# Kernel tuning notes

Hardware: AMD Instinct MI355X
Metric: run time of the kernel (lower is better)

Reference implementation:

```python
import jax, jax.numpy as jnp
import numpy as np

DIM = 256
HEADS = 8
WS = 7          # window_size
WN = 8          # window_num per side
H = W = WS * WN # 56
B = 32
MLP_HIDDEN = 4 * DIM
SCALE = (DIM // HEADS) ** -0.5
LN_EPS = 1e-5


def _rel_index(ws):
    # pairwise relative position index inside a ws x ws window (dense 0..(2ws-1)^2-1,
    # so remap_position_index is the identity relabeling)
    ch, cw = np.meshgrid(np.arange(ws), np.arange(ws), indexing='ij')
    cf = np.stack([ch.ravel(), cw.ravel()])            # (2, ws*ws)
    rel = cf[:, :, None] - cf[:, None, :]              # (2, N, N)
    rel = rel.transpose(1, 2, 0).astype(np.int32)
    rel[..., 0] += ws - 1
    rel[..., 1] += ws - 1
    rel[..., 0] *= 2 * ws - 1
    return rel.sum(-1)                                 # (N, N) in [0, (2ws-1)^2)


def _layernorm(x, g, b):
    m = x.mean(-1, keepdims=True)
    v = ((x - m) ** 2).mean(-1, keepdims=True)
    return (x - m) * jax.lax.rsqrt(v + LN_EPS) * g + b


def _mhsa(x, qkv_w, qkv_b, proj_w, proj_b, bias):
    # x: (B_, N, C); bias: (nH, N, N) or None
    B_, N, C = x.shape
    hd = C // HEADS
    qkv = (x @ qkv_w.T + qkv_b).reshape(B_, N, 3, HEADS, hd).transpose(2, 0, 3, 1, 4)
    q, k, v = qkv[0], qkv[1], qkv[2]
    attn = jnp.einsum('bhqd,bhkd->bhqk', q * SCALE, k)
    if bias is not None:
        attn = attn + bias[None]
    attn = jax.nn.softmax(attn, axis=-1)
    out = jnp.einsum('bhqk,bhkd->bhqd', attn, v).transpose(0, 2, 1, 3).reshape(B_, N, C)
    return out @ proj_w.T + proj_b


def setup_inputs() -> dict:
    key = jax.random.key(0)
    ks = jax.random.split(key, 8)
    f32 = jnp.float32
    return {
        'regional_tokens': jax.random.normal(ks[0], (B, WN * WN, DIM), f32),
        'x': jax.random.normal(ks[1], (B, H * W, DIM), f32),
        'norm1_g': jnp.ones((DIM,), f32), 'norm1_b': jnp.zeros((DIM,), f32),
        'norm2_g': jnp.ones((DIM,), f32), 'norm2_b': jnp.zeros((DIM,), f32),
        'norm3_g': jnp.ones((DIM,), f32), 'norm3_b': jnp.zeros((DIM,), f32),
        'qkv_w': jax.random.normal(ks[2], (3 * DIM, DIM), f32) * 0.02,
        'qkv_b': jnp.zeros((3 * DIM,), f32),
        'proj_w': jax.random.normal(ks[3], (DIM, DIM), f32) * 0.02,
        'proj_b': jnp.zeros((DIM,), f32),
        'bias_table': jax.random.normal(ks[4], ((2 * WS - 1) ** 2, HEADS), f32) * 0.02,
        'fc1_w': jax.random.normal(ks[5], (MLP_HIDDEN, DIM), f32) * 0.02,
        'fc1_b': jnp.zeros((MLP_HIDDEN,), f32),
        'fc2_w': jax.random.normal(ks[6], (DIM, MLP_HIDDEN), f32) * 0.02,
        'fc2_b': jnp.zeros((DIM,), f32),
        'rel_index': jnp.asarray(_rel_index(WS)),
    }


def reference(regional_tokens, x, norm1_g, norm1_b, norm2_g, norm2_b, norm3_g, norm3_b,
              qkv_w, qkv_b, proj_w, proj_b, bias_table, fc1_w, fc1_b, fc2_w, fc2_b,
              rel_index):
    Bb, L, C = x.shape
    nW = regional_tokens.shape[1]
    ws2 = WS * WS
    # --- RSA: attention over regional tokens (no relative bias) ---
    regional_tokens = regional_tokens + _mhsa(
        _layernorm(regional_tokens, norm1_g, norm1_b), qkv_w, qkv_b, proj_w, proj_b, None)
    # --- window partition of x: (B,H,W,C) -> (nW*B, ws*ws, C) (batch-major) ---
    xw = x.reshape(Bb, H // WS, WS, W // WS, WS, C)
    xw = xw.transpose(0, 1, 3, 2, 4, 5).reshape(-1, ws2, C)
    # regional tokens reshaped window-major, exactly as the torch code does
    reg = regional_tokens.transpose(1, 0, 2).reshape(nW * Bb, 1, C)
    t = jnp.concatenate([reg, xw], axis=1)  # (nW*B, 1+ws2, C)
    # --- LSA relative position bias, zero-padded for the regional token ---
    bias = bias_table[rel_index]                       # (ws2, ws2, nH)
    bias = jnp.pad(bias, ((1, 0), (1, 0), (0, 0)))      # (1+ws2, 1+ws2, nH)
    bias = bias.transpose(2, 0, 1)                      # (nH, N, N)
    t = t + _mhsa(_layernorm(t, norm2_g, norm2_b), qkv_w, qkv_b, proj_w, proj_b, bias)
    # --- MLP ---
    h = _layernorm(t, norm3_g, norm3_b)
    h = jax.nn.gelu(h @ fc1_w.T + fc1_b, approximate=False) @ fc2_w.T + fc2_b
    t = t + h
    # --- split back ---
    reg_out = t[:, 0, :].reshape(nW, Bb, C).transpose(1, 0, 2)   # (B, nW, C)
    xw = t[:, 1:, :].reshape(Bb, H // WS, W // WS, WS, WS, C)
    x_out = xw.transpose(0, 1, 3, 2, 4, 5).reshape(Bb, L, C)
    return reg_out, x_out
```

## Files before the change

### kernel.cpp

```cpp
#include <hip/hip_runtime.h>
#include <math.h>

#define SCALE_Q 0.17677669529663687f

typedef __attribute__((ext_vector_type(8))) short bf16x8;
typedef __attribute__((ext_vector_type(4))) float f32x4;
typedef __attribute__((ext_vector_type(4))) unsigned short u16x4;

static __device__ __forceinline__ unsigned short f2bf(float f) {
    unsigned int u = __float_as_uint(f);
    u += 0x7FFF + ((u >> 16) & 1);
    return (unsigned short)(u >> 16);
}

static __device__ __forceinline__ float gelu_fast(float v) {
    float s = v * (0.7978845608f + 0.0356774081f * v * v);
    float e = __expf(-2.0f * s);
    return v * __builtin_amdgcn_rcpf(1.0f + e);
}

__global__ void prep_kernel(const float* __restrict__ qkv_w, const float* __restrict__ proj_w,
                            const float* __restrict__ fc1_w, const float* __restrict__ fc2_w,
                            const float* __restrict__ bias_table, const int* __restrict__ rel_index,
                            unsigned short* __restrict__ wq, unsigned short* __restrict__ wp,
                            unsigned short* __restrict__ w1, unsigned short* __restrict__ w2,
                            float* __restrict__ bias_pad) {
    int tid = blockIdx.x * blockDim.x + threadIdx.x;
    int stride = gridDim.x * blockDim.x;
    for (int i = tid; i < 768 * 256; i += stride) wq[i] = f2bf(qkv_w[i]);
    for (int i = tid; i < 256 * 256; i += stride) wp[i] = f2bf(proj_w[i]);
    for (int i = tid; i < 1024 * 256; i += stride) w1[i] = f2bf(fc1_w[i]);
    for (int i = tid; i < 256 * 1024; i += stride) w2[i] = f2bf(fc2_w[i]);
    for (int i = tid; i < 8 * 64 * 64; i += stride) {
        int h = i >> 12, q = (i >> 6) & 63, k = i & 63;
        float v;
        if (k >= 50) v = -1e30f;
        else if (q == 0 || k == 0 || q >= 50) v = 0.f;
        else v = bias_table[rel_index[(q - 1) * 49 + (k - 1)] * 8 + h];
        bias_pad[i] = v;
    }
}

template <int IS_RSA>
__global__ __launch_bounds__(1024, 4) void attn_kernel(
    const float* __restrict__ reg_tok, const float* __restrict__ x,
    const float* __restrict__ reg2_in, float* __restrict__ out,
    const float* __restrict__ ln_g, const float* __restrict__ ln_b,
    const unsigned short* __restrict__ wq, const float* __restrict__ qkv_b,
    const unsigned short* __restrict__ wp, const float* __restrict__ proj_b,
    const float* __restrict__ bias_pad) {
    __shared__ __align__(16) unsigned char smem[140288];
    unsigned short* regA = (unsigned short*)smem;
    unsigned short* regB = (unsigned short*)(smem + 36864);
    unsigned short* vT   = (unsigned short*)(smem + 103424);

    const int tid = threadIdx.x;
    const int lane = tid & 63;
    const int wid = tid >> 6;
    const int l15 = lane & 15;
    const int lg = lane >> 4;
    const int u = blockIdx.x;
    const int NV = IS_RSA ? 64 : 50;
    const f32x4 fzero = {0.f, 0.f, 0.f, 0.f};

    int reg_off = 0, xb = 0, wi = 0, wj = 0;
    if (!IS_RSA) {
        reg_off = ((u & 31) * 64 + (u >> 5)) * 256;
        xb = u >> 6;
        int xn = u & 63;
        wi = xn >> 3; wj = xn & 7;
    }

    for (int r = wid; r < 64; r += 16) {
        if (r < NV) {
            const float* src;
            if (IS_RSA) src = reg_tok + (u * 64 + r) * 256;
            else if (r == 0) src = reg2_in + reg_off;
            else {
                int p = r - 1;
                src = x + (xb * 3136 + (wi * 7 + p / 7) * 56 + (wj * 7 + p % 7)) * 256;
            }
            f32x4 v = *(const f32x4*)(src + lane * 4);
            float s = v[0] + v[1] + v[2] + v[3];
            float s2 = v[0] * v[0] + v[1] * v[1] + v[2] * v[2] + v[3] * v[3];
            #pragma unroll
            for (int m = 1; m < 64; m <<= 1) { s += __shfl_xor(s, m); s2 += __shfl_xor(s2, m); }
            float mean = s * 0.00390625f;
            float rstd = rsqrtf(s2 * 0.00390625f - mean * mean + 1e-5f);
            u16x4 o;
            #pragma unroll
            for (int j = 0; j < 4; ++j) {
                int c = lane * 4 + j;
                o[j] = f2bf((v[j] - mean) * rstd * ln_g[c] + ln_b[c]);
            }
            *(u16x4*)(regA + r * 264 + lane * 4) = o;
        } else {
            u16x4 z = {0, 0, 0, 0};
            *(u16x4*)(regA + r * 264 + lane * 4) = z;
        }
    }
    __syncthreads();

    const int h = wid >> 1;
    const int qb = (wid & 1) * 32;

    {
        f32x4 acc[4][3];
        #pragma unroll
        for (int mi = 0; mi < 4; ++mi)
            #pragma unroll
            for (int t = 0; t < 3; ++t) acc[mi][t] = fzero;
        #pragma unroll
        for (int ks = 0; ks < 8; ++ks) {
            int k = ks * 32 + lg * 8;
            bf16x8 a[4], b[3];
            #pragma unroll
            for (int mi = 0; mi < 4; ++mi) a[mi] = *(const bf16x8*)(regA + (mi * 16 + l15) * 264 + k);
            #pragma unroll
            for (int t = 0; t < 3; ++t) b[t] = *(const bf16x8*)(wq + (wid * 48 + t * 16 + l15) * 256 + k);
            #pragma unroll
            for (int mi = 0; mi < 4; ++mi)
                #pragma unroll
                for (int t = 0; t < 3; ++t)
                    acc[mi][t] = __builtin_amdgcn_mfma_f32_16x16x32_bf16(a[mi], b[t], acc[mi][t], 0, 0, 0);
        }
        #pragma unroll
        for (int mi = 0; mi < 4; ++mi)
            #pragma unroll
            for (int t = 0; t < 3; ++t) {
                int col = wid * 48 + t * 16 + l15;
                float bias = qkv_b[col];
                #pragma unroll
                for (int r = 0; r < 4; ++r) {
                    int row = mi * 16 + lg * 4 + r;
                    unsigned short hv = f2bf(acc[mi][t][r] + bias);
                    if (col < 512) regB[row * 520 + col] = hv;
                    else vT[(col - 512) * 72 + row] = hv;
                }
            }
    }

    f32x4 bv[4][2];
    if (!IS_RSA) {
        #pragma unroll
        for (int mi = 0; mi < 4; ++mi)
            #pragma unroll
            for (int nj = 0; nj < 2; ++nj)
                bv[mi][nj] = *(const f32x4*)(bias_pad + h * 4096 + (qb + nj * 16 + l15) * 64 + mi * 16 + lg * 4);
    }
    __syncthreads();

    f32x4 st[4][2];
    {
        int k0 = h * 32 + lg * 8;
        bf16x8 af[4], bfq[2];
        #pragma unroll
        for (int mi = 0; mi < 4; ++mi) af[mi] = *(const bf16x8*)(regB + (mi * 16 + l15) * 520 + 256 + k0);
        #pragma unroll
        for (int nj = 0; nj < 2; ++nj) bfq[nj] = *(const bf16x8*)(regB + (qb + nj * 16 + l15) * 520 + k0);
        #pragma unroll
        for (int mi = 0; mi < 4; ++mi)
            #pragma unroll
            for (int nj = 0; nj < 2; ++nj)
                st[mi][nj] = __builtin_amdgcn_mfma_f32_16x16x32_bf16(af[mi], bfq[nj], fzero, 0, 0, 0);
    }

    u16x4 pf[4][2];
    #pragma unroll
    for (int nj = 0; nj < 2; ++nj) {
        float ps[4][4];
        float mx = -3.0e38f;
        #pragma unroll
        for (int mi = 0; mi < 4; ++mi)
            #pragma unroll
            for (int r = 0; r < 4; ++r) {
                float t = st[mi][nj][r] * SCALE_Q;
                if (!IS_RSA) t += bv[mi][nj][r];
                ps[mi][r] = t;
                mx = fmaxf(mx, t);
            }
        mx = fmaxf(mx, __shfl_xor(mx, 16));
        mx = fmaxf(mx, __shfl_xor(mx, 32));
        float sum = 0.f;
        #pragma unroll
        for (int mi = 0; mi < 4; ++mi)
            #pragma unroll
            for (int r = 0; r < 4; ++r) { ps[mi][r] = __expf(ps[mi][r] - mx); sum += ps[mi][r]; }
        sum += __shfl_xor(sum, 16);
        sum += __shfl_xor(sum, 32);
        float inv = __builtin_amdgcn_rcpf(sum);
        #pragma unroll
        for (int mi = 0; mi < 4; ++mi) {
            u16x4 p4;
            #pragma unroll
            for (int r = 0; r < 4; ++r) p4[r] = f2bf(ps[mi][r] * inv);
            pf[mi][nj] = p4;
        }
    }

    f32x4 ov[2][2];
    #pragma unroll
    for (int m2 = 0; m2 < 2; ++m2) { ov[m2][0] = fzero; ov[m2][1] = fzero; }
    #pragma unroll
    for (int kt = 0; kt < 4; ++kt) {
        bf16x8 pb[2];
        #pragma unroll
        for (int nj = 0; nj < 2; ++nj) {
            bf16x8 t;
            t[0] = (short)pf[kt][nj][0]; t[1] = (short)pf[kt][nj][1];
            t[2] = (short)pf[kt][nj][2]; t[3] = (short)pf[kt][nj][3];
            t[4] = 0; t[5] = 0; t[6] = 0; t[7] = 0;
            pb[nj] = t;
        }
        #pragma unroll
        for (int m2 = 0; m2 < 2; ++m2) {
            u16x4 av = *(const u16x4*)(vT + (h * 32 + m2 * 16 + l15) * 72 + kt * 16 + lg * 4);
            bf16x8 a8;
            a8[0] = (short)av[0]; a8[1] = (short)av[1]; a8[2] = (short)av[2]; a8[3] = (short)av[3];
            a8[4] = 0; a8[5] = 0; a8[6] = 0; a8[7] = 0;
            #pragma unroll
            for (int nj = 0; nj < 2; ++nj)
                ov[m2][nj] = __builtin_amdgcn_mfma_f32_16x16x32_bf16(a8, pb[nj], ov[m2][nj], 0, 0, 0);
        }
    }
    #pragma unroll
    for (int m2 = 0; m2 < 2; ++m2)
        #pragma unroll
        for (int nj = 0; nj < 2; ++nj) {
            u16x4 o4;
            #pragma unroll
            for (int r = 0; r < 4; ++r) o4[r] = f2bf(ov[m2][nj][r]);
            *(u16x4*)(regA + (qb + nj * 16 + l15) * 264 + h * 32 + m2 * 16 + lg * 4) = o4;
        }
    __syncthreads();

    {
        int nb = wid * 16;
        f32x4 acc[4];
        #pragma unroll
        for (int mi = 0; mi < 4; ++mi) acc[mi] = fzero;
        #pragma unroll
        for (int ks = 0; ks < 8; ++ks) {
            int k = ks * 32 + lg * 8;
            bf16x8 a[4], b;
            #pragma unroll
            for (int mi = 0; mi < 4; ++mi) a[mi] = *(const bf16x8*)(regA + (mi * 16 + l15) * 264 + k);
            b = *(const bf16x8*)(wp + (nb + l15) * 256 + k);
            #pragma unroll
            for (int mi = 0; mi < 4; ++mi)
                acc[mi] = __builtin_amdgcn_mfma_f32_16x16x32_bf16(a[mi], b, acc[mi], 0, 0, 0);
        }
        int col = nb + l15;
        float pb = proj_b[col];
        #pragma unroll
        for (int mi = 0; mi < 4; ++mi)
            #pragma unroll
            for (int r = 0; r < 4; ++r) {
                int row = mi * 16 + lg * 4 + r;
                if (row < NV) {
                    float val = acc[mi][r] + pb;
                    if (IS_RSA) {
                        int off = (u * 64 + row) * 256 + col;
                        out[off] = val + reg_tok[off];
                    } else if (row == 0) {
                        out[reg_off + col] = val + reg2_in[reg_off + col];
                    } else {
                        int p = row - 1;
                        int off = (xb * 3136 + (wi * 7 + p / 7) * 56 + (wj * 7 + p % 7)) * 256 + col;
                        out[524288 + off] = val + x[off];
                    }
                }
            }
    }
}

__global__ __launch_bounds__(512, 4) void mlp_kernel(
    float* __restrict__ dout,
    const float* __restrict__ ln_g, const float* __restrict__ ln_b,
    const unsigned short* __restrict__ w1, const float* __restrict__ b1,
    const unsigned short* __restrict__ w2, const float* __restrict__ b2) {
    __shared__ __align__(16) unsigned short xst[64 * 264];
    __shared__ __align__(16) unsigned short hld[2][64 * 136];
    const int tid = threadIdx.x;
    const int lane = tid & 63;
    const int wid = tid >> 6;
    const int l15 = lane & 15;
    const int lg = lane >> 4;
    const int row0 = blockIdx.x * 64;
    const f32x4 fzero = {0.f, 0.f, 0.f, 0.f};

    #pragma unroll
    for (int i = 0; i < 8; ++i) {
        int r = wid * 8 + i;
        f32x4 v = *(const f32x4*)(dout + (row0 + r) * 256 + lane * 4);
        float s = v[0] + v[1] + v[2] + v[3];
        float s2 = v[0] * v[0] + v[1] * v[1] + v[2] * v[2] + v[3] * v[3];
        #pragma unroll
        for (int m = 1; m < 64; m <<= 1) { s += __shfl_xor(s, m); s2 += __shfl_xor(s2, m); }
        float mean = s * 0.00390625f;
        float rstd = rsqrtf(s2 * 0.00390625f - mean * mean + 1e-5f);
        u16x4 o;
        #pragma unroll
        for (int j = 0; j < 4; ++j) {
            int c = lane * 4 + j;
            o[j] = f2bf((v[j] - mean) * rstd * ln_g[c] + ln_b[c]);
        }
        *(u16x4*)(xst + r * 264 + lane * 4) = o;
    }

    bf16x8 w1f[8], w2f[8];
    #pragma unroll
    for (int ks = 0; ks < 8; ++ks)
        w1f[ks] = *(const bf16x8*)(w1 + (wid * 16 + l15) * 256 + ks * 32 + lg * 8);
    #pragma unroll
    for (int ks = 0; ks < 4; ++ks)
        #pragma unroll
        for (int ni = 0; ni < 2; ++ni)
            w2f[ks * 2 + ni] = *(const bf16x8*)(w2 + (wid * 32 + ni * 16 + l15) * 1024 + ks * 32 + lg * 8);
    __syncthreads();

    f32x4 acc2[4][2];
    #pragma unroll
    for (int mi = 0; mi < 4; ++mi) { acc2[mi][0] = fzero; acc2[mi][1] = fzero; }

    #pragma unroll
    for (int c = 0; c < 8; ++c) {
        unsigned short* hb = &hld[c & 1][0];
        f32x4 acc1[4];
        #pragma unroll
        for (int mi = 0; mi < 4; ++mi) acc1[mi] = fzero;
        #pragma unroll
        for (int ks = 0; ks < 8; ++ks) {
            int k = ks * 32 + lg * 8;
            bf16x8 a[4];
            #pragma unroll
            for (int mi = 0; mi < 4; ++mi)
                a[mi] = *(const bf16x8*)(xst + (mi * 16 + l15) * 264 + k);
            #pragma unroll
            for (int mi = 0; mi < 4; ++mi)
                acc1[mi] = __builtin_amdgcn_mfma_f32_16x16x32_bf16(a[mi], w1f[ks], acc1[mi], 0, 0, 0);
        }
        if (c < 7) {
            #pragma unroll
            for (int ks = 0; ks < 8; ++ks)
                w1f[ks] = *(const bf16x8*)(w1 + ((c + 1) * 128 + wid * 16 + l15) * 256 + ks * 32 + lg * 8);
        }
        {
            int hc = wid * 16 + l15;
            float bb = b1[c * 128 + hc];
            #pragma unroll
            for (int mi = 0; mi < 4; ++mi)
                #pragma unroll
                for (int r = 0; r < 4; ++r)
                    hb[(mi * 16 + lg * 4 + r) * 136 + hc] = f2bf(gelu_fast(acc1[mi][r] + bb));
        }
        __syncthreads();
        #pragma unroll
        for (int ks = 0; ks < 4; ++ks) {
            int k = ks * 32 + lg * 8;
            bf16x8 a[4];
            #pragma unroll
            for (int mi = 0; mi < 4; ++mi)
                a[mi] = *(const bf16x8*)(hb + (mi * 16 + l15) * 136 + k);
            #pragma unroll
            for (int mi = 0; mi < 4; ++mi)
                #pragma unroll
                for (int ni = 0; ni < 2; ++ni)
                    acc2[mi][ni] = __builtin_amdgcn_mfma_f32_16x16x32_bf16(a[mi], w2f[ks * 2 + ni], acc2[mi][ni], 0, 0, 0);
        }
        if (c < 7) {
            #pragma unroll
            for (int ks = 0; ks < 4; ++ks)
                #pragma unroll
                for (int ni = 0; ni < 2; ++ni)
                    w2f[ks * 2 + ni] = *(const bf16x8*)(w2 + (wid * 32 + ni * 16 + l15) * 1024 + (c + 1) * 128 + ks * 32 + lg * 8);
        }
    }
    #pragma unroll
    for (int mi = 0; mi < 4; ++mi)
        #pragma unroll
        for (int ni = 0; ni < 2; ++ni) {
            int col = wid * 32 + ni * 16 + l15;
            float bb = b2[col];
            #pragma unroll
            for (int r = 0; r < 4; ++r) {
                int row = row0 + mi * 16 + lg * 4 + r;
                float* dst = dout + row * 256 + col;
                *dst = acc2[mi][ni][r] + bb + *dst;
            }
        }
}

extern "C" void kernel_launch(void* const* d_in, const int* in_sizes, int n_in,
                              void* d_out, int out_size, void* d_ws, size_t ws_size,
                              hipStream_t stream) {
    const float* regional = (const float*)d_in[0];
    const float* x = (const float*)d_in[1];
    const float* n1g = (const float*)d_in[2];
    const float* n1b = (const float*)d_in[3];
    const float* n2g = (const float*)d_in[4];
    const float* n2b = (const float*)d_in[5];
    const float* n3g = (const float*)d_in[6];
    const float* n3b = (const float*)d_in[7];
    const float* qkvw = (const float*)d_in[8];
    const float* qkvb = (const float*)d_in[9];
    const float* projw = (const float*)d_in[10];
    const float* projb = (const float*)d_in[11];
    const float* btab = (const float*)d_in[12];
    const float* f1w = (const float*)d_in[13];
    const float* f1b = (const float*)d_in[14];
    const float* f2w = (const float*)d_in[15];
    const float* f2b = (const float*)d_in[16];
    const int* relidx = (const int*)d_in[17];

    unsigned char* ws = (unsigned char*)d_ws;
    unsigned short* wq = (unsigned short*)(ws);
    unsigned short* wp = (unsigned short*)(ws + 393216);
    unsigned short* w1 = (unsigned short*)(ws + 524288);
    unsigned short* w2 = (unsigned short*)(ws + 1048576);
    float* bias_pad    = (float*)(ws + 1572864);
    float* reg2        = (float*)(ws + 1703936);

    float* out = (float*)d_out;

    prep_kernel<<<512, 256, 0, stream>>>(qkvw, projw, f1w, f2w, btab, relidx, wq, wp, w1, w2, bias_pad);
    attn_kernel<1><<<32, 1024, 0, stream>>>(regional, x, nullptr, reg2, n1g, n1b, wq, qkvb, wp, projb, nullptr);
    attn_kernel<0><<<2048, 1024, 0, stream>>>(regional, x, reg2, out, n2g, n2b, wq, qkvb, wp, projb, bias_pad);
    mlp_kernel<<<1600, 512, 0, stream>>>(out, n3g, n3b, w1, f1b, w2, f2b);
}
```

Measured before the change: 485.4 us.

## Use LDS-only barriers, prefetch proj weights, and uniform-branch QKV scatter

Replaces __syncthreads with a custom barrier that waits only on LDS/scalar counters, so outstanding global loads (weight prefetches) need not drain at each barrier. Projection weights are prefetched into registers right after the QKV GEMM so their latency overlaps attention. The QKV store is split into wave-uniform branches by q/k versus v, removing per-element divergence. The w2 fragment loads move inside the MLP loop just before the barrier, lowering register pressure at the cost of less prefetch distance.

Result: slower. 498.4 us (+2.7%).

```diff
diff --git a/kernel.cpp b/kernel.cpp
--- a/kernel.cpp
+++ b/kernel.cpp
@@ -17,6 +17,12 @@
     float s = v * (0.7978845608f + 0.0356774081f * v * v);
     float e = __expf(-2.0f * s);
     return v * __builtin_amdgcn_rcpf(1.0f + e);
+}
+
+static __device__ __forceinline__ void barrier_lds_only() {
+    asm volatile("s_waitcnt lgkmcnt(0)" ::: "memory");
+    __builtin_amdgcn_s_barrier();
+    asm volatile("" ::: "memory");
 }
 
 __global__ void prep_kernel(const float* __restrict__ qkv_w, const float* __restrict__ proj_w,
@@ -57,6 +63,7 @@
     const int tid = threadIdx.x;
     const int lane = tid & 63;
     const int wid = tid >> 6;
+    const int widu = __builtin_amdgcn_readfirstlane(wid);
     const int l15 = lane & 15;
     const int lg = lane >> 4;
     const int u = blockIdx.x;
@@ -99,11 +106,12 @@
             *(u16x4*)(regA + r * 264 + lane * 4) = z;
         }
     }
-    __syncthreads();
+    barrier_lds_only();
 
     const int h = wid >> 1;
     const int qb = (wid & 1) * 32;
 
+    bf16x8 wpf[8];
     {
         f32x4 acc[4][3];
         #pragma unroll
@@ -125,19 +133,34 @@
                     acc[mi][t] = __builtin_amdgcn_mfma_f32_16x16x32_bf16(a[mi], b[t], acc[mi][t], 0, 0, 0);
         }
         #pragma unroll
-        for (int mi = 0; mi < 4; ++mi)
-            #pragma unroll
-            for (int t = 0; t < 3; ++t) {
-                int col = wid * 48 + t * 16 + l15;
-                float bias = qkv_b[col];
+        for (int ks = 0; ks < 8; ++ks)
+            wpf[ks] = *(const bf16x8*)(wp + (wid * 16 + l15) * 256 + ks * 32 + lg * 8);
+        #pragma unroll
+        for (int t = 0; t < 3; ++t) {
+            if (3 * widu + t < 32) {
                 #pragma unroll
-                for (int r = 0; r < 4; ++r) {
-                    int row = mi * 16 + lg * 4 + r;
-                    unsigned short hv = f2bf(acc[mi][t][r] + bias);
-                    if (col < 512) regB[row * 520 + col] = hv;
-                    else vT[(col - 512) * 72 + row] = hv;
+                for (int mi = 0; mi < 4; ++mi) {
+                    int col = wid * 48 + t * 16 + l15;
+                    float bias = qkv_b[col];
+                    #pragma unroll
+                    for (int r = 0; r < 4; ++r) {
+                        int row = mi * 16 + lg * 4 + r;
+                        regB[row * 520 + col] = f2bf(acc[mi][t][r] + bias);
+                    }
                 }
-            }
+            } else {
+                #pragma unroll
+                for (int mi = 0; mi < 4; ++mi) {
+                    int col = wid * 48 + t * 16 + l15;
+                    float bias = qkv_b[col];
+                    #pragma unroll
+                    for (int r = 0; r < 4; ++r) {
+                        int row = mi * 16 + lg * 4 + r;
+                        vT[(col - 512) * 72 + row] = f2bf(acc[mi][t][r] + bias);
+                    }
+                }
+            }
+        }
     }
 
     f32x4 bv[4][2];
@@ -148,7 +171,7 @@
             for (int nj = 0; nj < 2; ++nj)
                 bv[mi][nj] = *(const f32x4*)(bias_pad + h * 4096 + (qb + nj * 16 + l15) * 64 + mi * 16 + lg * 4);
     }
-    __syncthreads();
+    barrier_lds_only();
 
     f32x4 st[4][2];
     {
@@ -232,25 +255,23 @@
             for (int r = 0; r < 4; ++r) o4[r] = f2bf(ov[m2][nj][r]);
             *(u16x4*)(regA + (qb + nj * 16 + l15) * 264 + h * 32 + m2 * 16 + lg * 4) = o4;
         }
-    __syncthreads();
+    barrier_lds_only();
 
     {
-        int nb = wid * 16;
         f32x4 acc[4];
         #pragma unroll
         for (int mi = 0; mi < 4; ++mi) acc[mi] = fzero;
         #pragma unroll
         for (int ks = 0; ks < 8; ++ks) {
             int k = ks * 32 + lg * 8;
-            bf16x8 a[4], b;
+            bf16x8 a[4];
             #pragma unroll
             for (int mi = 0; mi < 4; ++mi) a[mi] = *(const bf16x8*)(regA + (mi * 16 + l15) * 264 + k);
-            b = *(const bf16x8*)(wp + (nb + l15) * 256 + k);
-            #pragma unroll
-            for (int mi = 0; mi < 4; ++mi)
-                acc[mi] = __builtin_amdgcn_mfma_f32_16x16x32_bf16(a[mi], b, acc[mi], 0, 0, 0);
-        }
-        int col = nb + l15;
+            #pragma unroll
+            for (int mi = 0; mi < 4; ++mi)
+                acc[mi] = __builtin_amdgcn_mfma_f32_16x16x32_bf16(a[mi], wpf[ks], acc[mi], 0, 0, 0);
+        }
+        int col = wid * 16 + l15;
         float pb = proj_b[col];
         #pragma unroll
         for (int mi = 0; mi < 4; ++mi)
@@ -308,16 +329,11 @@
         *(u16x4*)(xst + r * 264 + lane * 4) = o;
     }
 
-    bf16x8 w1f[8], w2f[8];
+    bf16x8 w1f[8];
     #pragma unroll
     for (int ks = 0; ks < 8; ++ks)
         w1f[ks] = *(const bf16x8*)(w1 + (wid * 16 + l15) * 256 + ks * 32 + lg * 8);
-    #pragma unroll
-    for (int ks = 0; ks < 4; ++ks)
-        #pragma unroll
-        for (int ni = 0; ni < 2; ++ni)
-            w2f[ks * 2 + ni] = *(const bf16x8*)(w2 + (wid * 32 + ni * 16 + l15) * 1024 + ks * 32 + lg * 8);
-    __syncthreads();
+    barrier_lds_only();
 
     f32x4 acc2[4][2];
     #pragma unroll
@@ -354,7 +370,13 @@
                 for (int r = 0; r < 4; ++r)
                     hb[(mi * 16 + lg * 4 + r) * 136 + hc] = f2bf(gelu_fast(acc1[mi][r] + bb));
         }
-        __syncthreads();
+        bf16x8 w2f[8];
+        #pragma unroll
+        for (int ks = 0; ks < 4; ++ks)
+            #pragma unroll
+            for (int ni = 0; ni < 2; ++ni)
+                w2f[ks * 2 + ni] = *(const bf16x8*)(w2 + (wid * 32 + ni * 16 + l15) * 1024 + c * 128 + ks * 32 + lg * 8);
+        barrier_lds_only();
         #pragma unroll
         for (int ks = 0; ks < 4; ++ks) {
             int k = ks * 32 + lg * 8;
@@ -367,13 +389,6 @@
                 #pragma unroll
                 for (int ni = 0; ni < 2; ++ni)
                     acc2[mi][ni] = __builtin_amdgcn_mfma_f32_16x16x32_bf16(a[mi], w2f[ks * 2 + ni], acc2[mi][ni], 0, 0, 0);
-        }
-        if (c < 7) {
-            #pragma unroll
-            for (int ks = 0; ks < 4; ++ks)
-                #pragma unroll
-                for (int ni = 0; ni < 2; ++ni)
-                    w2f[ks * 2 + ni] = *(const bf16x8*)(w2 + (wid * 32 + ni * 16 + l15) * 1024 + (c + 1) * 128 + ks * 32 + lg * 8);
         }
     }
     #pragma unroll
```
